# Kernel tuning notes

Measured on AMD Instinct MI355X. Metric: run time of the kernel, lower is better.

Reference implementation:

```python
import jax, jax.numpy as jnp
import numpy as np

IN_CHANS = 64
OUT_CHANS = 64
IN_SHAPE = (128, 128)
RADIUS_CUTOFF = 0.03
KERNEL_SHAPE = (3, 4)  # (n_rings, n_phi) -> (3-1)*4+1 = 9 basis functions
EPS = 1e-5
NEG_SLOPE = 0.2


def _disco_basis():
    """Dynamically compile the DISCO filter basis on the (2H, 2W) equidistant grid.

    Returns psi of shape [K, kh, kw] (K=9 hat-function basis filters, including
    quadrature weight hx*hy) plus the pixel radii (Ry, Rx) of the support.
    All static -> constant-folded under jit.
    """
    H2, W2 = 2 * IN_SHAPE[0], 2 * IN_SHAPE[1]
    r_cut = RADIUS_CUTOFF / 2.0
    hy, hx = 1.0 / H2, 1.0 / W2            # normalized grid spacing
    Ry = int(np.ceil(r_cut / hy))
    Rx = int(np.ceil(r_cut / hx))
    dy = np.arange(-Ry, Ry + 1)[:, None] * hy
    dx = np.arange(-Rx, Rx + 1)[None, :] * hx
    r = np.sqrt(dy * dy + dx * dx)
    phi = np.arctan2(dy, dx) % (2.0 * np.pi)
    nr, nphi = KERNEL_SHAPE
    K = (nr - 1) * nphi + 1
    dr = r_cut / (nr - 1)
    dphi = 2.0 * np.pi / nphi
    ik = np.arange(K)[:, None, None]
    ir = np.where(ik > 0, (ik - 1) // nphi + 1, 0)   # radial ring index
    iphi = (ik - 1) % nphi                            # angular index
    # radial hat functions centered at ir*dr, clipped at the cutoff radius
    r_val = np.where((np.abs(r - ir * dr) <= dr) & (r <= r_cut),
                     1.0 - np.abs(r - ir * dr) / dr, 0.0)
    # periodic angular hat functions centered at iphi*dphi
    d_ang = np.abs(phi - iphi * dphi)
    d_ang = np.minimum(d_ang, 2.0 * np.pi - d_ang)
    phi_val = np.where(d_ang <= dphi, 1.0 - d_ang / dphi, 0.0)
    psi = np.where(ik == 0, r_val, r_val * phi_val)   # center basis is isotropic
    psi = psi * (hx * hy)                              # quadrature weight
    return jnp.asarray(psi, jnp.float32), Ry, Rx


def _upsample2x_align_corners(x):
    """Bilinear 2x upsample with align_corners=True, x: [N, C, H, W]."""
    N, C, H, W = x.shape

    def axis(n):
        no = 2 * n
        s = jnp.arange(no, dtype=jnp.float32) * (n - 1) / (no - 1)
        i0 = jnp.floor(s).astype(jnp.int32)
        i1 = jnp.minimum(i0 + 1, n - 1)
        w = (s - i0).astype(x.dtype)
        return i0, i1, w

    y0, y1, wy = axis(H)
    x = x[:, :, y0, :] * (1.0 - wy)[None, None, :, None] + x[:, :, y1, :] * wy[None, None, :, None]
    x0, x1, wx = axis(W)
    x = x[:, :, :, x0] * (1.0 - wx) + x[:, :, :, x1] * wx
    return x


def setup_inputs() -> dict:
    key = jax.random.key(0)
    k1, k2 = jax.random.split(key)
    image = jax.random.normal(k1, (4, IN_CHANS, IN_SHAPE[0], IN_SHAPE[1]), dtype=jnp.float32)
    K = (KERNEL_SHAPE[0] - 1) * KERNEL_SHAPE[1] + 1
    scale = 1.0 / np.sqrt(IN_CHANS * K)
    weight = jax.random.normal(k2, (OUT_CHANS, IN_CHANS, K), dtype=jnp.float32) * scale
    return {"image": image, "weight": weight}


def reference(image, weight):
    x = _upsample2x_align_corners(image)  # [N, Cin, 2H, 2W]
    # 2) DISCO conv: contract learned weights with compiled basis -> dense filter
    psi, Ry, Rx = _disco_basis()          # [K, kh, kw]
    kernel = jnp.einsum('oik,khw->oihw', weight, psi)
    y = jax.lax.conv_general_dilated(
        x, kernel, window_strides=(1, 1),
        padding=[(Ry, Ry), (Rx, Rx)],       # 'constant' zero padding, same size
        dimension_numbers=('NCHW', 'OIHW', 'NCHW'))
    # 3) InstanceNorm2d (affine=False, biased variance, eps=1e-5)
    mu = jnp.mean(y, axis=(2, 3), keepdims=True)
    var = jnp.var(y, axis=(2, 3), keepdims=True)
    y = (y - mu) * jax.lax.rsqrt(var + EPS)
    # 4) LeakyReLU(0.2)
    return jnp.where(y >= 0, y, NEG_SLOPE * y)
```

## Files before the change

kernel.cpp:

```cpp
#include <hip/hip_runtime.h>

#define NB 4
#define CIN 64
#define COUT 64
#define H 128
#define W 128
#define H2 256
#define W2 256
#define HS 24

#define WS_W    0
#define WS_P1   32768
#define WS_P2   98304
#define WS_MU   163840
#define WS_RSTD 164096

constexpr double csqrt(double x) {
    double g = x > 1.0 ? x : 1.0;
    for (int i = 0; i < 64; ++i) g = 0.5 * (g + x / g);
    return g;
}
constexpr double catan_pos(double x) {
    double f = 1.0;
    for (int i = 0; i < 6; ++i) { x = x / (1.0 + csqrt(1.0 + x * x)); f *= 2.0; }
    double x2 = x * x, s = 0.0, term = x;
    for (int n = 0; n < 10; ++n) { s += term / (2 * n + 1) * ((n & 1) ? -1.0 : 1.0); term *= x2; }
    return f * s;
}
constexpr double catan2c(double y, double x) {
    const double PI = 3.141592653589793;
    if (x == 0.0 && y == 0.0) return 0.0;
    double ax = x < 0 ? -x : x, ay = y < 0 ? -y : y;
    double a = (ax >= ay) ? catan_pos(ay / ax) : (PI / 2.0 - catan_pos(ax / ay));
    if (x < 0) a = PI - a;
    return (y < 0) ? -a : a;
}

struct PsiTab { double v[81][9]; };
constexpr PsiTab compute_psi() {
    PsiTab P{};
    const double hy = 1.0 / 256.0;
    const double rcut = 0.015;
    const double dr = 0.0075;
    const double PI = 3.141592653589793;
    const double TWO_PI = 6.283185307179586;
    const double dphi = PI / 2.0;
    for (int ky = 0; ky < 9; ++ky)
        for (int kx = 0; kx < 9; ++kx) {
            double dy = (double)(ky - 4) * hy;
            double dx = (double)(kx - 4) * hy;
            double r = csqrt(dy * dy + dx * dx);
            double phi = catan2c(dy, dx);
            if (phi < 0.0) phi += TWO_PI;
            for (int k = 0; k < 9; ++k) {
                int ir = (k == 0) ? 0 : ((k - 1) / 4 + 1);
                double ctr = ir * dr;
                double ad = r > ctr ? r - ctr : ctr - r;
                double rv = (ad <= dr && r <= rcut) ? 1.0 - ad / dr : 0.0;
                double val;
                if (k == 0) val = rv;
                else {
                    int ip = (k - 1) % 4;
                    double da = phi - ip * dphi; if (da < 0) da = -da;
                    double d2 = TWO_PI - da; if (d2 < da) da = d2;
                    double pv = (da <= dphi) ? 1.0 - da / dphi : 0.0;
                    val = rv * pv;
                }
                P.v[ky * 9 + kx][k] = val * (hy * hy);
            }
        }
    return P;
}

struct TapTab {
    int nt;
    int off[48];
    float val[48][9];
    bool nz[48][9];
};
constexpr TapTab make_taps() {
    TapTab T{};
    PsiTab P = compute_psi();
    for (int ky = 0; ky < 9; ++ky)
        for (int kx = 0; kx < 9; ++kx) {
            int t = ky * 9 + kx;
            bool any = false;
            for (int k = 0; k < 9; ++k) if (P.v[t][k] != 0.0) any = true;
            if (!any) continue;
            int dy = ky - 4, dx = kx - 4;
            T.off[T.nt] = dy * HS + dx;
            for (int k = 0; k < 9; ++k) {
                T.val[T.nt][k] = (float)P.v[t][k];
                T.nz[T.nt][k] = (P.v[t][k] != 0.0);
            }
            T.nt++;
        }
    return T;
}
constexpr TapTab TT = make_taps();
constexpr int NT = TT.nt;
static_assert(NT > 0 && NT <= 48, "tap table overflow");

using f32x2  = __attribute__((ext_vector_type(2))) float;
using f32x4  = __attribute__((ext_vector_type(4))) float;
using bf16x8 = __attribute__((ext_vector_type(8))) short;

__device__ __forceinline__ unsigned short f2bf_rne(float f) {
    unsigned u = __float_as_uint(f);
    unsigned r = (u + 0x7fff + ((u >> 16) & 1)) >> 16;
    return (unsigned short)r;
}
__device__ __forceinline__ unsigned pkrtz(float a, float b) {
    return (__float_as_uint(a) >> 16) | (__float_as_uint(b) & 0xffff0000u);
}

__global__ void setup_w(const float* __restrict__ wgt, float* __restrict__ ws) {
    unsigned short* wsW = (unsigned short*)(ws + WS_W);
    const int g = blockIdx.x;
    const int t = threadIdx.x;
    const int o = t >> 2;
    const int k0 = (t & 3) * 8;
#pragma unroll
    for (int j = 0; j < 8; ++j) {
        int kk = k0 + j;
        int ch = kk >> 4, k = kk & 15;
        float v = (k < 9) ? wgt[((size_t)o * CIN + 2 * g + ch) * 9 + k] : 0.f;
        wsW[g * 2048 + o * 32 + kk] = f2bf_rne(v);
    }
}

__global__ __launch_bounds__(256, 2) void conv_kernel(const float* __restrict__ img,
                                                      float* __restrict__ out,
                                                      float* __restrict__ ws) {
    __shared__ unsigned short zbuf[256][40];
    __shared__ unsigned halo[2][22 * HS];
    __shared__ float red1[4][64], red2[4][64];

    const int tid  = threadIdx.x;
    const int bid  = blockIdx.x;
    const int n    = bid >> 8;
    const int tile = bid & 255;
    const int ty0  = (tile >> 4) << 4;
    const int tx0  = (tile & 15) << 4;

    const int r = tid >> 4, c = tid & 15;
    const int hbase = (r + 3) * HS + (c + 3);
    const int wv  = tid >> 6;
    const int l   = tid & 63;
    const int a16 = l & 15;
    const int kseg = (l >> 4) * 8;

    const unsigned short* wsW = (const unsigned short*)(ws + WS_W);

    {
        uint4* zr = (uint4*)&zbuf[0][0];
#pragma unroll
        for (int j = 0; j < 5; ++j) zr[tid + j * 256] = make_uint4(0, 0, 0, 0);
    }

    const float cs = (float)(127.0 / 255.0);

    float Lr[2][8];
    float sFY[2], sFX[2];
    int   sIdx[2];
    bool  sZF[2];

    auto stage_issue = [&](int g) {
        const float* im0 = img + ((size_t)n * CIN + 2 * g) * (H * W);
        const float* im1 = im0 + H * W;
#pragma unroll
        for (int j = 0; j < 2; ++j) {
            int e = tid + j * 256;
            if (e < 484) {
                int hy = e / 22, hx = e - hy * 22;
                int uy = ty0 - 3 + hy, ux = tx0 - 3 + hx;
                bool zf = ((unsigned)uy >= 256u) || ((unsigned)ux >= 256u);
                float syf = (float)uy * cs;
                float sxf = (float)ux * cs;
                int y0 = (int)syf; y0 = min(max(y0, 0), 127);
                int x0 = (int)sxf; x0 = min(max(x0, 0), 127);
                int y1 = min(y0 + 1, 127), x1 = min(x0 + 1, 127);
                sFY[j] = syf - (float)y0;
                sFX[j] = sxf - (float)x0;
                sIdx[j] = hy * HS + hx;
                sZF[j] = zf;
                int b00 = y0 * W + x0, b01 = y0 * W + x1;
                int b10 = y1 * W + x0, b11 = y1 * W + x1;
                Lr[j][0] = im0[b00]; Lr[j][1] = im0[b01];
                Lr[j][2] = im0[b10]; Lr[j][3] = im0[b11];
                Lr[j][4] = im1[b00]; Lr[j][5] = im1[b01];
                Lr[j][6] = im1[b10]; Lr[j][7] = im1[b11];
            }
        }
    };
    auto stage_commit = [&](int b) {
#pragma unroll
        for (int j = 0; j < 2; ++j) {
            int e = tid + j * 256;
            if (e < 484) {
                float fy = sFY[j], fx = sFX[j];
                float t0 = Lr[j][0] + fy * (Lr[j][2] - Lr[j][0]);
                float t1 = Lr[j][1] + fy * (Lr[j][3] - Lr[j][1]);
                float v0 = t0 + fx * (t1 - t0);
                float u0 = Lr[j][4] + fy * (Lr[j][6] - Lr[j][4]);
                float u1 = Lr[j][5] + fy * (Lr[j][7] - Lr[j][5]);
                float v1 = u0 + fx * (u1 - u0);
                if (sZF[j]) { v0 = 0.f; v1 = 0.f; }
                halo[b][sIdx[j]] = (unsigned)f2bf_rne(v0) | ((unsigned)f2bf_rne(v1) << 16);
            }
        }
    };

    auto zphase = [&](int b) {
        const unsigned* hb = &halo[b][0];
        f32x2 z[9];
#pragma unroll
        for (int k = 0; k < 9; ++k) z[k] = (f32x2){0.f, 0.f};
#pragma unroll
        for (int t = 0; t < NT; ++t) {
            unsigned d = hb[hbase + TT.off[t]];
            f32x2 h = (f32x2){__uint_as_float(d << 16), __uint_as_float(d & 0xffff0000u)};
#pragma unroll
            for (int k = 0; k < 9; ++k)
                if (TT.nz[t][k]) z[k] += h * TT.val[t][k];
        }
        *(uint4*)&zbuf[tid][0] = make_uint4(pkrtz(z[0].x, z[1].x), pkrtz(z[2].x, z[3].x),
                                            pkrtz(z[4].x, z[5].x), pkrtz(z[6].x, z[7].x));
        *(unsigned*)&zbuf[tid][8] = __float_as_uint(z[8].x) >> 16;
        *(uint4*)&zbuf[tid][16] = make_uint4(pkrtz(z[0].y, z[1].y), pkrtz(z[2].y, z[3].y),
                                             pkrtz(z[4].y, z[5].y), pkrtz(z[6].y, z[7].y));
        *(unsigned*)&zbuf[tid][24] = __float_as_uint(z[8].y) >> 16;
    };

    f32x4 acc[4][4];
#pragma unroll
    for (int m = 0; m < 4; ++m)
#pragma unroll
        for (int t = 0; t < 4; ++t) acc[m][t] = (f32x4){0.f, 0.f, 0.f, 0.f};

    stage_issue(0);
    stage_commit(0);
    int cur = 0;

#pragma unroll 1
    for (int g = 0; g < 32; ++g) {
        __syncthreads();
        bf16x8 af[4];
        {
            const unsigned short* wp = wsW + g * 2048 + a16 * 32 + kseg;
#pragma unroll
            for (int m = 0; m < 4; ++m)
                af[m] = *(const bf16x8*)(wp + m * 512);
        }
        if (g < 31) stage_issue(g + 1);
        zphase(cur);
        if (g < 31) stage_commit(cur ^ 1);
        __syncthreads();

        bf16x8 bfr[4];
#pragma unroll
        for (int t = 0; t < 4; ++t)
            bfr[t] = *(const bf16x8*)&zbuf[wv * 64 + t * 16 + a16][kseg];
#pragma unroll
        for (int m = 0; m < 4; ++m)
#pragma unroll
            for (int t = 0; t < 4; ++t)
                acc[m][t] = __builtin_amdgcn_mfma_f32_16x16x32_bf16(af[m], bfr[t], acc[m][t], 0, 0, 0);
        cur ^= 1;
    }

#pragma unroll
    for (int m = 0; m < 4; ++m) {
#pragma unroll
        for (int r4 = 0; r4 < 4; ++r4) {
            float s = 0.f, q = 0.f;
#pragma unroll
            for (int t = 0; t < 4; ++t) {
                float v = acc[m][t][r4];
                s += v; q = fmaf(v, v, q);
            }
#pragma unroll
            for (int msk = 1; msk < 16; msk <<= 1) {
                s += __shfl_xor(s, msk);
                q += __shfl_xor(q, msk);
            }
            if (a16 == 0) {
                int o = m * 16 + (l >> 4) * 4 + r4;
                red1[wv][o] = s;
                red2[wv][o] = q;
            }
        }
    }

    const size_t nbase = (size_t)n * COUT * (H2 * W2);
#pragma unroll
    for (int m = 0; m < 4; ++m)
#pragma unroll
        for (int t = 0; t < 4; ++t) {
            int Y = ty0 + wv * 4 + t;
            int X = tx0 + a16;
#pragma unroll
            for (int r4 = 0; r4 < 4; ++r4) {
                int o = m * 16 + (l >> 4) * 4 + r4;
                out[nbase + (size_t)o * (H2 * W2) + Y * W2 + X] = acc[m][t][r4];
            }
        }
    __syncthreads();
    if (tid < 64) {
        float S1 = red1[0][tid] + red1[1][tid] + red1[2][tid] + red1[3][tid];
        float S2 = red2[0][tid] + red2[1][tid] + red2[2][tid] + red2[3][tid];
        ws[WS_P1 + (n * COUT + tid) * 256 + tile] = S1;
        ws[WS_P2 + (n * COUT + tid) * 256 + tile] = S2;
    }
}

__global__ void stats_kernel(float* __restrict__ ws) {
    const int co  = blockIdx.x;
    const int tid = threadIdx.x;
    float s1 = ws[WS_P1 + co * 256 + tid];
    float s2 = ws[WS_P2 + co * 256 + tid];
#pragma unroll
    for (int m = 1; m < 64; m <<= 1) { s1 += __shfl_xor(s1, m); s2 += __shfl_xor(s2, m); }
    __shared__ float r1[4], r2[4];
    if ((tid & 63) == 0) { r1[tid >> 6] = s1; r2[tid >> 6] = s2; }
    __syncthreads();
    if (tid == 0) {
        float S1 = r1[0] + r1[1] + r1[2] + r1[3];
        float S2 = r2[0] + r2[1] + r2[2] + r2[3];
        const float inv = 1.f / 65536.f;
        float mu  = S1 * inv;
        float var = S2 * inv - mu * mu;
        ws[WS_MU + co]   = mu;
        ws[WS_RSTD + co] = 1.f / sqrtf(var + 1e-5f);
    }
}

__global__ void norm_kernel(float* __restrict__ out, const float* __restrict__ ws) {
    const int total = NB * COUT * H2 * W2 / 4;
    for (int idx = blockIdx.x * blockDim.x + threadIdx.x; idx < total;
         idx += gridDim.x * blockDim.x) {
        int co = idx >> 14;
        float mu = ws[WS_MU + co];
        float rs = ws[WS_RSTD + co];
        float4 v = ((float4*)out)[idx];
        float* p = (float*)&v;
#pragma unroll
        for (int j = 0; j < 4; ++j) {
            float t = (p[j] - mu) * rs;
            p[j] = (t >= 0.f) ? t : 0.2f * t;
        }
        ((float4*)out)[idx] = v;
    }
}

extern "C" void kernel_launch(void* const* d_in, const int* in_sizes, int n_in,
                              void* d_out, int out_size, void* d_ws, size_t ws_size,
                              hipStream_t stream) {
    const float* img = (const float*)d_in[0];
    const float* wgt = (const float*)d_in[1];
    float* out = (float*)d_out;
    float* ws  = (float*)d_ws;

    setup_w<<<32, 256, 0, stream>>>(wgt, ws);
    conv_kernel<<<NB * 256, 256, 0, stream>>>(img, out, ws);
    stats_kernel<<<256, 256, 0, stream>>>(ws);
    norm_kernel<<<2048, 256, 0, stream>>>(out, ws);
}
```

Baseline: 185.9 us.

## Double-buffer the z staging tile to drop one barrier per channel group

Adds a second zbuf buffer so each channel-group iteration needs one __syncthreads instead of two. It also raises launch bounds from 2 to 3 blocks per CU, cuts the zbuf row stride from 40 to 36 with uint2 loads, and fuses the split global-load/commit staging into one step. The aim is less barrier stall, higher occupancy and fewer LDS bank conflicts. In exchange it uses more LDS, gives up hiding global-load latency behind the z-phase, and the tighter register budget may cause spills.

Result: slower. 380.4 us (+104.7%).

```diff
diff --git a/kernel.cpp b/kernel.cpp
--- a/kernel.cpp
+++ b/kernel.cpp
@@ -8,6 +8,7 @@
 #define H2 256
 #define W2 256
 #define HS 24
+#define ZS 36
 
 #define WS_W    0
 #define WS_P1   32768
@@ -129,10 +130,10 @@
     }
 }
 
-__global__ __launch_bounds__(256, 2) void conv_kernel(const float* __restrict__ img,
+__global__ __launch_bounds__(256, 3) void conv_kernel(const float* __restrict__ img,
                                                       float* __restrict__ out,
                                                       float* __restrict__ ws) {
-    __shared__ unsigned short zbuf[256][40];
+    __shared__ unsigned short zbuf[2][256][ZS];
     __shared__ unsigned halo[2][22 * HS];
     __shared__ float red1[4][64], red2[4][64];
 
@@ -153,19 +154,14 @@
     const unsigned short* wsW = (const unsigned short*)(ws + WS_W);
 
     {
-        uint4* zr = (uint4*)&zbuf[0][0];
-#pragma unroll
-        for (int j = 0; j < 5; ++j) zr[tid + j * 256] = make_uint4(0, 0, 0, 0);
+        uint4* zr = (uint4*)&zbuf[0][0][0];
+#pragma unroll
+        for (int j = 0; j < 9; ++j) zr[tid + j * 256] = make_uint4(0, 0, 0, 0);
     }
 
     const float cs = (float)(127.0 / 255.0);
 
-    float Lr[2][8];
-    float sFY[2], sFX[2];
-    int   sIdx[2];
-    bool  sZF[2];
-
-    auto stage_issue = [&](int g) {
+    auto stage = [&](int g, int q) {
         const float* im0 = img + ((size_t)n * CIN + 2 * g) * (H * W);
         const float* im1 = im0 + H * W;
 #pragma unroll
@@ -180,71 +176,67 @@
                 int y0 = (int)syf; y0 = min(max(y0, 0), 127);
                 int x0 = (int)sxf; x0 = min(max(x0, 0), 127);
                 int y1 = min(y0 + 1, 127), x1 = min(x0 + 1, 127);
-                sFY[j] = syf - (float)y0;
-                sFX[j] = sxf - (float)x0;
-                sIdx[j] = hy * HS + hx;
-                sZF[j] = zf;
+                float fy = syf - (float)y0;
+                float fx = sxf - (float)x0;
                 int b00 = y0 * W + x0, b01 = y0 * W + x1;
                 int b10 = y1 * W + x0, b11 = y1 * W + x1;
-                Lr[j][0] = im0[b00]; Lr[j][1] = im0[b01];
-                Lr[j][2] = im0[b10]; Lr[j][3] = im0[b11];
-                Lr[j][4] = im1[b00]; Lr[j][5] = im1[b01];
-                Lr[j][6] = im1[b10]; Lr[j][7] = im1[b11];
+                float p00 = im0[b00], p01 = im0[b01], p10 = im0[b10], p11 = im0[b11];
+                float q00 = im1[b00], q01 = im1[b01], q10 = im1[b10], q11 = im1[b11];
+                float t0 = p00 + fy * (p10 - p00);
+                float t1 = p01 + fy * (p11 - p01);
+                float v0 = t0 + fx * (t1 - t0);
+                float u0 = q00 + fy * (q10 - q00);
+                float u1 = q01 + fy * (q11 - q01);
+                float v1 = u0 + fx * (u1 - u0);
+                if (zf) { v0 = 0.f; v1 = 0.f; }
+                halo[q][hy * HS + hx] = (unsigned)f2bf_rne(v0) | ((unsigned)f2bf_rne(v1) << 16);
             }
         }
     };
-    auto stage_commit = [&](int b) {
-#pragma unroll
-        for (int j = 0; j < 2; ++j) {
-            int e = tid + j * 256;
-            if (e < 484) {
-                float fy = sFY[j], fx = sFX[j];
-                float t0 = Lr[j][0] + fy * (Lr[j][2] - Lr[j][0]);
-                float t1 = Lr[j][1] + fy * (Lr[j][3] - Lr[j][1]);
-                float v0 = t0 + fx * (t1 - t0);
-                float u0 = Lr[j][4] + fy * (Lr[j][6] - Lr[j][4]);
-                float u1 = Lr[j][5] + fy * (Lr[j][7] - Lr[j][5]);
-                float v1 = u0 + fx * (u1 - u0);
-                if (sZF[j]) { v0 = 0.f; v1 = 0.f; }
-                halo[b][sIdx[j]] = (unsigned)f2bf_rne(v0) | ((unsigned)f2bf_rne(v1) << 16);
-            }
-        }
+
+    auto zphase = [&](int q, int p) {
+        const unsigned* hb = &halo[q][hbase - 75];
+        f32x2 z[9];
+#pragma unroll
+        for (int k = 0; k < 9; ++k) z[k] = (f32x2){0.f, 0.f};
+#pragma unroll
+        for (int t = 0; t < NT; ++t) {
+            unsigned d = hb[75 + TT.off[t]];
+            float lo = __uint_as_float(d << 16);
+            float hi = __uint_as_float(d & 0xffff0000u);
+#pragma unroll
+            for (int k = 0; k < 9; ++k)
+                if (TT.nz[t][k]) {
+                    z[k].x = fmaf(TT.val[t][k], lo, z[k].x);
+                    z[k].y = fmaf(TT.val[t][k], hi, z[k].y);
+                }
+        }
+        unsigned short* zr = &zbuf[p][tid][0];
+        ((uint2*)zr)[0] = make_uint2(pkrtz(z[0].x, z[1].x), pkrtz(z[2].x, z[3].x));
+        ((uint2*)zr)[1] = make_uint2(pkrtz(z[4].x, z[5].x), pkrtz(z[6].x, z[7].x));
+        zr[8] = (unsigned short)(__float_as_uint(z[8].x) >> 16);
+        ((uint2*)(zr + 16))[0] = make_uint2(pkrtz(z[0].y, z[1].y), pkrtz(z[2].y, z[3].y));
+        ((uint2*)(zr + 16))[1] = make_uint2(pkrtz(z[4].y, z[5].y), pkrtz(z[6].y, z[7].y));
+        zr[24] = (unsigned short)(__float_as_uint(z[8].y) >> 16);
     };
 
-    auto zphase = [&](int b) {
-        const unsigned* hb = &halo[b][0];
-        f32x2 z[9];
-#pragma unroll
-        for (int k = 0; k < 9; ++k) z[k] = (f32x2){0.f, 0.f};
-#pragma unroll
-        for (int t = 0; t < NT; ++t) {
-            unsigned d = hb[hbase + TT.off[t]];
-            f32x2 h = (f32x2){__uint_as_float(d << 16), __uint_as_float(d & 0xffff0000u)};
-#pragma unroll
-            for (int k = 0; k < 9; ++k)
-                if (TT.nz[t][k]) z[k] += h * TT.val[t][k];
-        }
-        *(uint4*)&zbuf[tid][0] = make_uint4(pkrtz(z[0].x, z[1].x), pkrtz(z[2].x, z[3].x),
-                                            pkrtz(z[4].x, z[5].x), pkrtz(z[6].x, z[7].x));
-        *(unsigned*)&zbuf[tid][8] = __float_as_uint(z[8].x) >> 16;
-        *(uint4*)&zbuf[tid][16] = make_uint4(pkrtz(z[0].y, z[1].y), pkrtz(z[2].y, z[3].y),
-                                             pkrtz(z[4].y, z[5].y), pkrtz(z[6].y, z[7].y));
-        *(unsigned*)&zbuf[tid][24] = __float_as_uint(z[8].y) >> 16;
-    };
-
     f32x4 acc[4][4];
 #pragma unroll
     for (int m = 0; m < 4; ++m)
 #pragma unroll
         for (int t = 0; t < 4; ++t) acc[m][t] = (f32x4){0.f, 0.f, 0.f, 0.f};
 
-    stage_issue(0);
-    stage_commit(0);
-    int cur = 0;
+    stage(0, 0);
+    int p = 0;
 
 #pragma unroll 1
     for (int g = 0; g < 32; ++g) {
+        if (g > 0) {
+        }
+        if (g < 31) stage(g + 1, p ^ 1);
+        zphase(p, p);
         __syncthreads();
+
         bf16x8 af[4];
         {
             const unsigned short* wp = wsW + g * 2048 + a16 * 32 + kseg;
@@ -252,21 +244,19 @@
             for (int m = 0; m < 4; ++m)
                 af[m] = *(const bf16x8*)(wp + m * 512);
         }
-        if (g < 31) stage_issue(g + 1);
-        zphase(cur);
-        if (g < 31) stage_commit(cur ^ 1);
-        __syncthreads();
-
-        bf16x8 bfr[4];
-#pragma unroll
-        for (int t = 0; t < 4; ++t)
-            bfr[t] = *(const bf16x8*)&zbuf[wv * 64 + t * 16 + a16][kseg];
+        union { uint2 q2[2]; bf16x8 v; } bfr[4];
+#pragma unroll
+        for (int t = 0; t < 4; ++t) {
+            const unsigned short* zp = &zbuf[p][wv * 64 + t * 16 + a16][kseg];
+            bfr[t].q2[0] = *(const uint2*)zp;
+            bfr[t].q2[1] = *(const uint2*)(zp + 4);
+        }
 #pragma unroll
         for (int m = 0; m < 4; ++m)
 #pragma unroll
             for (int t = 0; t < 4; ++t)
-                acc[m][t] = __builtin_amdgcn_mfma_f32_16x16x32_bf16(af[m], bfr[t], acc[m][t], 0, 0, 0);
-        cur ^= 1;
+                acc[m][t] = __builtin_amdgcn_mfma_f32_16x16x32_bf16(af[m], bfr[t].v, acc[m][t], 0, 0, 0);
+        p ^= 1;
     }
 
 #pragma unroll
```
